# Kernel tuning notes

Measured on AMD Instinct MI355X. Metric: run time of the kernel, lower is better.

Reference implementation:

```python
import jax, jax.numpy as jnp
import numpy as np

NG = 1024      # graphs
NPG = 128      # nodes per graph (forced by lin1 = Linear(128*hid, 128))
N = NG * NPG   # 131072 nodes
DEG = 16       # avg in-graph degree
E = N * DEG    # 2,097,152 edges
IN, H = 4, 64


def setup_inputs() -> dict:
    key = jax.random.key(0)
    ks = jax.random.split(key, 24)
    x = jax.random.normal(ks[0], (N, IN), jnp.float32)
    # edges constrained within each 128-node graph
    src = jax.random.randint(ks[1], (E,), 0, NPG)
    dst = jax.random.randint(ks[2], (E,), 0, NPG)
    off = jnp.repeat(jnp.arange(NG, dtype=jnp.int32) * NPG, NPG * DEG)
    edge_index = jnp.stack([src.astype(jnp.int32) + off, dst.astype(jnp.int32) + off])
    g = lambda k, shp, fan: jax.random.normal(k, shp, jnp.float32) / np.float32(np.sqrt(fan))
    return {
        "x": x, "edge_index": edge_index,
        # GATv2Conv(4->64)
        "Wl": g(ks[3], (IN, H), IN), "bl": jnp.zeros((H,), jnp.float32),
        "Wr": g(ks[4], (IN, H), IN), "br": jnp.zeros((H,), jnp.float32),
        "att_v2": g(ks[5], (H,), H), "b_v2": jnp.zeros((H,), jnp.float32),
        # GATConv #1 (64->64)
        "Wg1": g(ks[6], (H, H), H), "as1": g(ks[7], (H,), H),
        "ad1": g(ks[8], (H,), H), "bg1": jnp.zeros((H,), jnp.float32),
        # GATConv #2 (64->64)
        "Wg2": g(ks[9], (H, H), H), "as2": g(ks[10], (H,), H),
        "ad2": g(ks[11], (H,), H), "bg2": jnp.zeros((H,), jnp.float32),
        # LayerNorm(64)
        "ln_g": jnp.ones((H,), jnp.float32), "ln_b": jnp.zeros((H,), jnp.float32),
        # heads: Linear(128*64 -> 128), Linear(128 -> 1)
        "W1": g(ks[12], (NPG * H, 128), NPG * H), "b1": jnp.zeros((128,), jnp.float32),
        "W2": g(ks[13], (128, 1), 128), "b2": jnp.zeros((1,), jnp.float32),
    }


def _seg_softmax(logits, seg):
    # stable softmax over edges grouped by destination node
    m = jax.ops.segment_max(logits, seg, num_segments=N)
    ex = jnp.exp(logits - m[seg])
    s = jax.ops.segment_sum(ex, seg, num_segments=N)
    return ex / (s[seg] + 1e-16)


def _gatv2(x, src, dst, Wl, bl, Wr, br, att, bias):
    xl = x @ Wl + bl                       # source transform [N,H]
    xr = x @ Wr + br                       # target transform [N,H]
    e = jax.nn.leaky_relu(xl[src] + xr[dst], 0.2) @ att   # [E]
    a = _seg_softmax(e, dst)
    out = jax.ops.segment_sum(a[:, None] * xl[src], dst, num_segments=N)
    return out + bias


def _gat(x, src, dst, W, a_src, a_dst, bias):
    # GATConv default: add self-loops
    loop = jnp.arange(N, dtype=src.dtype)
    s2 = jnp.concatenate([src, loop]); d2 = jnp.concatenate([dst, loop])
    xw = x @ W                             # [N,H]
    al_s = xw @ a_src; al_d = xw @ a_dst   # per-node attention halves [N]
    e = jax.nn.leaky_relu(al_s[s2] + al_d[d2], 0.2)
    a = _seg_softmax(e, d2)
    out = jax.ops.segment_sum(a[:, None] * xw[s2], d2, num_segments=N)
    return out + bias


def _layernorm(x, g, b, eps=1e-5):
    mu = jnp.mean(x, -1, keepdims=True)
    var = jnp.mean(jnp.square(x - mu), -1, keepdims=True)
    return (x - mu) * jax.lax.rsqrt(var + eps) * g + b


def reference(x, edge_index, Wl, bl, Wr, br, att_v2, b_v2,
              Wg1, as1, ad1, bg1, Wg2, as2, ad2, bg2,
              ln_g, ln_b, W1, b1, W2, b2):
    src, dst = edge_index[0], edge_index[1]
    h = jax.nn.leaky_relu(_gatv2(x, src, dst, Wl, bl, Wr, br, att_v2, b_v2), 0.01)
    h = _layernorm(h, ln_g, ln_b)
    h = jax.nn.relu(_gat(h, src, dst, Wg1, as1, ad1, bg1))
    h = jax.nn.relu(_gat(h, src, dst, Wg2, as2, ad2, bg2))
    # linearize: batch is sorted with exactly NPG nodes per graph -> reshape
    h = h.reshape(NG, NPG * H)
    h = jax.nn.leaky_relu(h @ W1 + b1, 0.01)
    return jax.nn.sigmoid(h @ W2 + b2)     # [NG, 1]
```

## Files before the change

kernel.cpp:

```cpp
#include <hip/hip_runtime.h>
#include <hip/hip_bf16.h>

#define NGRAPH 1024
#define NPG 128
#define EPG 2048
#define ETOT (NGRAPH*NPG*16)

typedef unsigned int uint;
typedef unsigned short ushort_t;
typedef __attribute__((ext_vector_type(8))) short s8v;
typedef __attribute__((ext_vector_type(4))) float f32x4;

#define MFMA16 __builtin_amdgcn_mfma_f32_16x16x32_bf16

__device__ __forceinline__ float lrelu(float x, float s){ return fmaxf(x, x*s); }
__device__ __forceinline__ float b2lo(uint u){ return __uint_as_float(u << 16); }
__device__ __forceinline__ float b2hi(uint u){ return __uint_as_float(u & 0xFFFF0000u); }
__device__ __forceinline__ uint pkbf(float a, float b){
  union { __hip_bfloat162 h; uint u; } t;
  t.h = __hip_bfloat162{__float2bfloat16(a), __float2bfloat16(b)};
  return t.u;
}
__device__ __forceinline__ ushort_t bfb(float v){
  union { __hip_bfloat16 h; ushort_t u; } t; t.h = __float2bfloat16(v); return t.u;
}
union U4S8 { uint4 u; s8v s; };
__device__ __forceinline__ s8v bcs8(uint4 u){ U4S8 t; t.u = u; return t.s; }
#define DPP_ADD(v, ctrl) ((v) + __int_as_float(__builtin_amdgcn_update_dpp(0, __float_as_int(v), (ctrl), 0xF, 0xF, false)))

__device__ __forceinline__ int oswz(int r, int p){ return (r<<5) | ((((p>>2) ^ (r & 7))<<2) | (p & 3)); }
__device__ __forceinline__ int obase(int r, int oc){ return (r<<5) | (((oc) ^ (r & 7))<<2); }

__device__ __forceinline__ void fma8(float* acc, uint4 q, float a){
  acc[0] += a*b2lo(q.x); acc[1] += a*b2hi(q.x);
  acc[2] += a*b2lo(q.y); acc[3] += a*b2hi(q.y);
  acc[4] += a*b2lo(q.z); acc[5] += a*b2hi(q.z);
  acc[6] += a*b2lo(q.w); acc[7] += a*b2hi(q.w);
}

#define O_A   0
#define O_B   4096
#define O_EVA 8192
#define O_ED  10240
#define O_WS  11264
#define O_SOF 11392
#define O_ALS 11457
#define O_ALD 11585
#define SM_SZ 11713

__global__ __launch_bounds__(256, 3) void gnn_fused(
    const float* __restrict__ x, const int* __restrict__ ei,
    const float* __restrict__ Wl, const float* __restrict__ bl,
    const float* __restrict__ Wr, const float* __restrict__ br,
    const float* __restrict__ att, const float* __restrict__ bv2,
    const float* __restrict__ Wg1, const float* __restrict__ as1,
    const float* __restrict__ ad1, const float* __restrict__ bg1,
    const float* __restrict__ Wg2, const float* __restrict__ as2,
    const float* __restrict__ ad2, const float* __restrict__ bg2,
    const float* __restrict__ lng, const float* __restrict__ lnb,
    uint* __restrict__ hout)
{
  __shared__ uint SM[SM_SZ];
  float*    eva    = (float*)(SM + O_EVA);
  ushort_t* edsL   = (ushort_t*)(SM + O_ED);
  ushort_t* soff16 = (ushort_t*)(SM + O_SOF);
  float*    als    = (float*)(SM + O_ALS);
  float*    ald    = (float*)(SM + O_ALD);
  float*    was    = (float*)(SM + O_WS);
  float*    wad    = was + 64;
  ushort_t* wgA16  = (ushort_t*)(SM + O_A);
  ushort_t* wg16   = (ushort_t*)(SM + O_EVA);

  const int g    = blockIdx.x;
  const int tid  = threadIdx.x;
  const int lane = tid & 63;
  const int wv   = tid >> 6;
  const int lw   = lane & 15;
  const int lq   = lane >> 4;
  const int sl   = lane & 7;
  const int grp  = lane >> 3;
  const int ebase = g * EPG;

  {
    int* spos = (int*)(SM + O_EVA);
    if (tid < NPG) spos[tid] = 0;
    __syncthreads();
    for (int e = tid; e < EPG; e += 256)
      atomicAdd(&spos[ei[ETOT + ebase + e] - g*NPG], 1);
    __syncthreads();
    if (wv == 0) {
      int c0 = spos[lane], c1 = spos[lane + 64];
      #pragma unroll
      for (int o = 1; o < 64; o <<= 1) { int t = __shfl_up(c0, o); if (lane >= o) c0 += t; }
      #pragma unroll
      for (int o = 1; o < 64; o <<= 1) { int t = __shfl_up(c1, o); if (lane >= o) c1 += t; }
      int tot0 = __shfl(c0, 63);
      soff16[lane + 1]  = (ushort_t)c0;
      soff16[lane + 65] = (ushort_t)(c1 + tot0);
      if (lane == 0) soff16[0] = 0;
    }
    __syncthreads();
    if (tid < NPG) spos[tid] = soff16[tid];
    __syncthreads();
    for (int e = tid; e < EPG; e += 256) {
      int s = ei[ebase + e] - g*NPG;
      int d = ei[ETOT + ebase + e] - g*NPG;
      int p = atomicAdd(&spos[d], 1);
      edsL[p] = (ushort_t)(s | (d << 8));
    }
  }

  {
    const int pl = lane & 31, hb = lane >> 5;
    const float2 wl0 = *(const float2*)&Wl[0*64 + 2*pl];
    const float2 wl1 = *(const float2*)&Wl[1*64 + 2*pl];
    const float2 wl2 = *(const float2*)&Wl[2*64 + 2*pl];
    const float2 wl3 = *(const float2*)&Wl[3*64 + 2*pl];
    const float2 wr0 = *(const float2*)&Wr[0*64 + 2*pl];
    const float2 wr1 = *(const float2*)&Wr[1*64 + 2*pl];
    const float2 wr2 = *(const float2*)&Wr[2*64 + 2*pl];
    const float2 wr3 = *(const float2*)&Wr[3*64 + 2*pl];
    const float2 blp = *(const float2*)&bl[2*pl];
    const float2 brp = *(const float2*)&br[2*pl];
    const float4* x4 = (const float4*)x + (size_t)g * NPG;
    for (int st = 0; st < 16; st++) {
      int i = st*8 + wv*2 + hb;
      float4 xi = x4[i];
      float l0 = blp.x + xi.x*wl0.x + xi.y*wl1.x + xi.z*wl2.x + xi.w*wl3.x;
      float l1 = blp.y + xi.x*wl0.y + xi.y*wl1.y + xi.z*wl2.y + xi.w*wl3.y;
      float r0 = brp.x + xi.x*wr0.x + xi.y*wr1.x + xi.z*wr2.x + xi.w*wr3.x;
      float r1 = brp.y + xi.x*wr0.y + xi.y*wr1.y + xi.z*wr2.y + xi.w*wr3.y;
      SM[O_A + oswz(i, pl)] = pkbf(l0, l1);
      SM[O_B + oswz(i, pl)] = pkbf(r0, r1);
    }
  }
  __syncthreads();

  {
    float4 atA = *(const float4*)&att[sl*8];
    float4 atB = *(const float4*)&att[sl*8 + 4];
    float4 bvA = *(const float4*)&bv2[sl*8];
    float4 bvB = *(const float4*)&bv2[sl*8 + 4];
    for (int pass = 0; pass < 4; pass++) {
      int d  = wv*32 + pass*8 + grp;
      int p0 = soff16[d], p1 = soff16[d+1];
      uint4 qr = *(uint4*)&SM[O_B + obase(d, sl)];
      float m = -1e30f;
      if (p0 < p1) {
        int sN = edsL[p0] & 127;
        uint4 qN = *(uint4*)&SM[O_A + obase(sN, sl)];
        for (int e = p0; e < p1; e++) {
          uint4 ql = qN;
          if (e + 1 < p1) { sN = edsL[e+1] & 127; qN = *(uint4*)&SM[O_A + obase(sN, sl)]; }
          float pt;
          pt  = lrelu(b2lo(ql.x)+b2lo(qr.x), 0.2f)*atA.x;
          pt += lrelu(b2hi(ql.x)+b2hi(qr.x), 0.2f)*atA.y;
          pt += lrelu(b2lo(ql.y)+b2lo(qr.y), 0.2f)*atA.z;
          pt += lrelu(b2hi(ql.y)+b2hi(qr.y), 0.2f)*atA.w;
          pt += lrelu(b2lo(ql.z)+b2lo(qr.z), 0.2f)*atB.x;
          pt += lrelu(b2hi(ql.z)+b2hi(qr.z), 0.2f)*atB.y;
          pt += lrelu(b2lo(ql.w)+b2lo(qr.w), 0.2f)*atB.z;
          pt += lrelu(b2hi(ql.w)+b2hi(qr.w), 0.2f)*atB.w;
          pt += __shfl_xor(pt, 1); pt += __shfl_xor(pt, 2); pt += __shfl_xor(pt, 4);
          if (sl == 0) eva[e] = pt;
          m = fmaxf(m, pt);
        }
      }
      float ss = 0.f;
      for (int e = p0 + sl; e < p1; e += 8) ss += __expf(eva[e] - m);
      ss += __shfl_xor(ss, 1); ss += __shfl_xor(ss, 2); ss += __shfl_xor(ss, 4);
      float rnm = 1.f / (ss + 1e-16f);
      float acc[8] = {0,0,0,0,0,0,0,0};
      if (p0 < p1) {
        int sN = edsL[p0] & 127;
        uint4 qN = *(uint4*)&SM[O_A + obase(sN, sl)];
        float evN = eva[p0];
        for (int e = p0; e < p1; e++) {
          uint4 ql = qN; float ev = evN;
          if (e + 1 < p1) {
            sN = edsL[e+1] & 127;
            qN = *(uint4*)&SM[O_A + obase(sN, sl)];
            evN = eva[e+1];
          }
          fma8(acc, ql, __expf(ev - m) * rnm);
        }
      }
      uint4 o;
      o.x = pkbf(lrelu(acc[0]+bvA.x,0.01f), lrelu(acc[1]+bvA.y,0.01f));
      o.y = pkbf(lrelu(acc[2]+bvA.z,0.01f), lrelu(acc[3]+bvA.w,0.01f));
      o.z = pkbf(lrelu(acc[4]+bvB.x,0.01f), lrelu(acc[5]+bvB.y,0.01f));
      o.w = pkbf(lrelu(acc[6]+bvB.z,0.01f), lrelu(acc[7]+bvB.w,0.01f));
      *(uint4*)&SM[O_B + obase(d, sl)] = o;
    }
  }
  __syncthreads();

  {
    int pl = lane & 31, hb = lane >> 5;
    float2 gv = *(const float2*)&lng[2*pl];
    float2 bv = *(const float2*)&lnb[2*pl];
    for (int it = 0; it < 16; it++) {
      int d = it*8 + wv*2 + hb;
      uint w = SM[O_B + oswz(d, pl)];
      float v0 = b2lo(w), v1 = b2hi(w);
      float s1 = v0 + v1, s2 = v0*v0 + v1*v1;
      #pragma unroll
      for (int o = 1; o < 32; o <<= 1) { s1 += __shfl_xor(s1, o); s2 += __shfl_xor(s2, o); }
      float mu  = s1 * 0.015625f;
      float var = s2 * 0.015625f - mu*mu;
      float rs  = rsqrtf(var + 1e-5f);
      SM[O_B + oswz(d, pl)] = pkbf((v0-mu)*rs*gv.x + bv.x, (v1-mu)*rs*gv.y + bv.y);
    }
  }
  __syncthreads();

  for (int layer = 0; layer < 2; layer++) {
    const float* Wg  = layer ? Wg2 : Wg1;
    const float* avs = layer ? as2 : as1;
    const float* avd = layer ? ad2 : ad1;
    const float* bg  = layer ? bg2 : bg1;

    if (tid < 128) {
      const float* av = (tid < 64) ? avs : avd;
      float* dst = (tid < 64) ? was : wad;
      int k = tid & 63;
      float acc = 0.f;
      #pragma unroll
      for (int jj = 0; jj < 16; jj++) {
        float4 w = *(const float4*)&Wg[k*64 + jj*4];
        float4 a = *(const float4*)&av[jj*4];
        acc += w.x*a.x + w.y*a.y + w.z*a.z + w.w*a.w;
      }
      dst[k] = acc;
    } else {
      int t2 = tid - 128;
      #pragma unroll
      for (int i = 0; i < 8; i++) {
        int idx = t2 + i*128;
        int k = idx >> 4, j4 = (idx & 15)*4;
        float4 w = *(const float4*)&Wg[k*64 + j4];
        wg16[oswz(j4+0, k>>1)*2 + (k&1)] = bfb(w.x);
        wg16[oswz(j4+1, k>>1)*2 + (k&1)] = bfb(w.y);
        wg16[oswz(j4+2, k>>1)*2 + (k&1)] = bfb(w.z);
        wg16[oswz(j4+3, k>>1)*2 + (k&1)] = bfb(w.w);
      }
    }
    __syncthreads();

    {
      int row = 16*wv + lw;
      s8v a0 = bcs8(*(uint4*)&SM[O_EVA + obase(row, lq)]);
      s8v a1 = bcs8(*(uint4*)&SM[O_EVA + obase(row, 4+lq)]);
      int j0 = 16*wv + lq*4;
      #pragma unroll
      for (int nt = 0; nt < 8; nt++) {
        int d = nt*16 + lw;
        s8v b0 = bcs8(*(uint4*)&SM[O_B + obase(d, lq)]);
        s8v b1 = bcs8(*(uint4*)&SM[O_B + obase(d, 4+lq)]);
        f32x4 c = {0.f,0.f,0.f,0.f};
        c = MFMA16(a0, b0, c, 0, 0, 0);
        c = MFMA16(a1, b1, c, 0, 0, 0);
        #pragma unroll
        for (int rg = 0; rg < 4; rg++) {
          int j = j0 + rg;
          wgA16[oswz(d, j>>1)*2 + (j&1)] = bfb(c[rg]);
        }
      }
      float4 ws0 = *(float4*)&was[sl*8], ws1 = *(float4*)&was[sl*8 + 4];
      float4 wd0 = *(float4*)&wad[sl*8], wd1 = *(float4*)&wad[sl*8 + 4];
      for (int ps = 0; ps < 4; ps++) {
        int n = ps*32 + (tid >> 3);
        uint4 q = *(uint4*)&SM[O_B + obase(n, sl)];
        float f0=b2lo(q.x), f1=b2hi(q.x), f2=b2lo(q.y), f3=b2hi(q.y);
        float f4=b2lo(q.z), f5=b2hi(q.z), f6=b2lo(q.w), f7=b2hi(q.w);
        float sa = f0*ws0.x+f1*ws0.y+f2*ws0.z+f3*ws0.w+f4*ws1.x+f5*ws1.y+f6*ws1.z+f7*ws1.w;
        float sd = f0*wd0.x+f1*wd0.y+f2*wd0.z+f3*wd0.w+f4*wd1.x+f5*wd1.y+f6*wd1.z+f7*wd1.w;
        sa = DPP_ADD(sa, 0x111); sa = DPP_ADD(sa, 0x112); sa = DPP_ADD(sa, 0x114);
        sd = DPP_ADD(sd, 0x111); sd = DPP_ADD(sd, 0x112); sd = DPP_ADD(sd, 0x114);
        if ((lane & 7) == 7) { als[n] = sa; ald[n] = sd; }
      }
    }
    __syncthreads();

    {
      float4 bgA = *(const float4*)&bg[sl*8];
      float4 bgB = *(const float4*)&bg[sl*8 + 4];
      for (int pass = 0; pass < 4; pass++) {
        int d  = wv*32 + pass*8 + grp;
        int p0 = soff16[d], p1 = soff16[d+1];
        float ald_d = ald[d];
        float lgs = lrelu(als[d] + ald_d, 0.2f);
        float m = lgs;
        for (int e = p0 + sl; e < p1; e += 8)
          m = fmaxf(m, lrelu(als[edsL[e] & 127] + ald_d, 0.2f));
        m = fmaxf(m, __shfl_xor(m, 1)); m = fmaxf(m, __shfl_xor(m, 2)); m = fmaxf(m, __shfl_xor(m, 4));
        float ex0 = __expf(lgs - m);
        float ss = (sl == 0) ? ex0 : 0.f;
        for (int e = p0 + sl; e < p1; e += 8)
          ss += __expf(lrelu(als[edsL[e] & 127] + ald_d, 0.2f) - m);
        ss += __shfl_xor(ss, 1); ss += __shfl_xor(ss, 2); ss += __shfl_xor(ss, 4);
        float rnm = 1.f / (ss + 1e-16f);
        float acc[8] = {0,0,0,0,0,0,0,0};
        fma8(acc, *(uint4*)&SM[O_A + obase(d, sl)], ex0 * rnm);
        if (p0 < p1) {
          int sN = edsL[p0] & 127;
          float alN = als[sN];
          uint4 qN = *(uint4*)&SM[O_A + obase(sN, sl)];
          for (int e = p0; e < p1; e++) {
            uint4 ql = qN; float alv = alN;
            if (e + 1 < p1) {
              sN = edsL[e+1] & 127;
              alN = als[sN];
              qN = *(uint4*)&SM[O_A + obase(sN, sl)];
            }
            fma8(acc, ql, __expf(lrelu(alv + ald_d, 0.2f) - m) * rnm);
          }
        }
        uint4 o;
        o.x = pkbf(fmaxf(acc[0]+bgA.x,0.f), fmaxf(acc[1]+bgA.y,0.f));
        o.y = pkbf(fmaxf(acc[2]+bgA.z,0.f), fmaxf(acc[3]+bgA.w,0.f));
        o.z = pkbf(fmaxf(acc[4]+bgB.x,0.f), fmaxf(acc[5]+bgB.y,0.f));
        o.w = pkbf(fmaxf(acc[6]+bgB.z,0.f), fmaxf(acc[7]+bgB.w,0.f));
        *(uint4*)&SM[O_B + obase(d, sl)] = o;
      }
    }
    __syncthreads();
  }

  {
    uint* hg = hout + (size_t)g * 4096;
    #pragma unroll
    for (int i = 0; i < 16; i++) {
      int idx = tid + i*256;
      hg[idx] = SM[O_B + oswz(idx >> 5, idx & 31)];
    }
  }
}

__global__ __launch_bounds__(256) void w1_transpose(const float* __restrict__ W1,
                                                    uint* __restrict__ w1t)
{
  __shared__ float sw[64*130];
  const int tid = threadIdx.x;
  const int k0 = blockIdx.x * 64;
  #pragma unroll
  for (int i = 0; i < 8; i++) {
    int idx = tid + i*256;
    int r = idx >> 5, c4 = (idx & 31)*4;
    *(float4*)&sw[r*130 + c4] = *(const float4*)&W1[(size_t)(k0+r)*128 + c4];
  }
  __syncthreads();
  #pragma unroll
  for (int i = 0; i < 16; i++) {
    int idx = tid + i*256;
    int c = idx >> 5, kp = idx & 31;
    w1t[(size_t)c*4096 + (k0>>1) + kp] = pkbf(sw[(2*kp)*130 + c], sw[(2*kp+1)*130 + c]);
  }
}

__global__ __launch_bounds__(256) void head_gemm(
    const uint* __restrict__ hbuf, const uint* __restrict__ w1t,
    float* __restrict__ partial)
{
  __shared__ uint sAh[2048];
  __shared__ uint sBh[4096];
  const int tid = threadIdx.x, lane = tid & 63, wv = tid >> 6;
  const int lw = lane & 15, lq = lane >> 4;
  const int g0 = blockIdx.x * 64;
  const int ks = blockIdx.y;
  f32x4 acc[8];
  #pragma unroll
  for (int i = 0; i < 8; i++) acc[i] = f32x4{0.f,0.f,0.f,0.f};

  for (int ch = 0; ch < 8; ch++) {
    int pb = ks*256 + ch*32;
    #pragma unroll
    for (int i = 0; i < 2; i++) {
      int idx = tid + i*256; int r = idx >> 3, q4 = idx & 7;
      uint4 v = *(const uint4*)&hbuf[(size_t)(g0+r)*4096 + pb + q4*4];
      *(uint4*)&sAh[(r<<5) | ((q4 ^ (r & 7))<<2)] = v;
    }
    #pragma unroll
    for (int i = 0; i < 4; i++) {
      int idx = tid + i*256; int r = idx >> 3, q4 = idx & 7;
      uint4 v = *(const uint4*)&w1t[(size_t)r*4096 + pb + q4*4];
      *(uint4*)&sBh[(r<<5) | ((q4 ^ (r & 7))<<2)] = v;
    }
    __syncthreads();
    int ra = 16*wv + lw;
    s8v a0 = bcs8(*(uint4*)&sAh[obase(ra, lq)]);
    s8v a1 = bcs8(*(uint4*)&sAh[obase(ra, 4+lq)]);
    #pragma unroll
    for (int nt = 0; nt < 8; nt++) {
      int c = nt*16 + lw;
      s8v b0 = bcs8(*(uint4*)&sBh[obase(c, lq)]);
      s8v b1 = bcs8(*(uint4*)&sBh[obase(c, 4+lq)]);
      acc[nt] = MFMA16(a0, b0, acc[nt], 0, 0, 0);
      acc[nt] = MFMA16(a1, b1, acc[nt], 0, 0, 0);
    }
    __syncthreads();
  }
  float* pp = partial + (size_t)ks*131072;
  #pragma unroll
  for (int nt = 0; nt < 8; nt++) {
    int c = nt*16 + lw;
    int r0 = g0 + 16*wv + lq*4;
    #pragma unroll
    for (int rg = 0; rg < 4; rg++)
      pp[(size_t)(r0+rg)*128 + c] = acc[nt][rg];
  }
}

__global__ __launch_bounds__(256) void head_out(
    const float* __restrict__ partial, const float* __restrict__ b1,
    const float* __restrict__ W2, const float* __restrict__ b2,
    float* __restrict__ out)
{
  const int tid = threadIdx.x;
  const int gl  = tid >> 5;
  const int c4  = tid & 31;
  const int g   = blockIdx.x*8 + gl;
  float4 v = *(const float4*)&b1[c4*4];
  #pragma unroll
  for (int s = 0; s < 16; s++) {
    float4 p = *(const float4*)&partial[(size_t)s*131072 + (size_t)g*128 + c4*4];
    v.x += p.x; v.y += p.y; v.z += p.z; v.w += p.w;
  }
  float4 w = *(const float4*)&W2[c4*4];
  float t = lrelu(v.x,0.01f)*w.x + lrelu(v.y,0.01f)*w.y
          + lrelu(v.z,0.01f)*w.z + lrelu(v.w,0.01f)*w.w;
  #pragma unroll
  for (int m = 1; m < 32; m <<= 1) t += __shfl_xor(t, m);
  if (c4 == 0) out[g] = 1.f / (1.f + __expf(-(t + b2[0])));
}

extern "C" void kernel_launch(void* const* d_in, const int* in_sizes, int n_in,
                              void* d_out, int out_size, void* d_ws, size_t ws_size,
                              hipStream_t stream) {
  const float* x   = (const float*)d_in[0];
  const int*   ei  = (const int*)  d_in[1];
  const float* Wl  = (const float*)d_in[2];
  const float* bl_ = (const float*)d_in[3];
  const float* Wr  = (const float*)d_in[4];
  const float* br_ = (const float*)d_in[5];
  const float* att = (const float*)d_in[6];
  const float* bv2 = (const float*)d_in[7];
  const float* Wg1 = (const float*)d_in[8];
  const float* as1 = (const float*)d_in[9];
  const float* ad1 = (const float*)d_in[10];
  const float* bg1 = (const float*)d_in[11];
  const float* Wg2 = (const float*)d_in[12];
  const float* as2 = (const float*)d_in[13];
  const float* ad2 = (const float*)d_in[14];
  const float* bg2 = (const float*)d_in[15];
  const float* lng = (const float*)d_in[16];
  const float* lnb = (const float*)d_in[17];
  const float* W1  = (const float*)d_in[18];
  const float* b1  = (const float*)d_in[19];
  const float* W2  = (const float*)d_in[20];
  const float* b2  = (const float*)d_in[21];
  float* out = (float*)d_out;

  uint*  hbuf    = (uint*)d_ws;
  float* partial = (float*)((char*)d_ws + (size_t)16*1024*1024);
  uint*  w1t     = (uint*)((char*)d_ws + (size_t)24*1024*1024);

  w1_transpose<<<128, 256, 0, stream>>>(W1, w1t);
  gnn_fused<<<NGRAPH, 256, 0, stream>>>(x, ei, Wl, bl_, Wr, br_, att, bv2,
      Wg1, as1, ad1, bg1, Wg2, as2, ad2, bg2, lng, lnb, hbuf);
  head_gemm<<<dim3(16, 16), 256, 0, stream>>>(hbuf, w1t, partial);
  head_out<<<128, 256, 0, stream>>>(partial, b1, W2, b2, out);
}
```

Measured before the change: 314.7 us.

## Switch GNN to fp16 with dot2, edge-parallel attention logits, drop W1 transpose kernel

Moves all intermediate storage and MFMA inputs from bf16 to fp16, so packed fp16 math (fdot2, half2 add and mul) can compute the GATv2 logits, the LayerNorm sums and the attention halves. Attention logits are now computed edge-parallel across all threads into a shared buffer. A separate segment-softmax pass then stores exponentials and per-node reciprocal sums, so the aggregation loops only do weighted FMAs and apply the normalizer once at the end. The separate W1 transpose kernel is removed and head_gemm converts and transposes W1 from fp32 itself on every tile load, trading a launch for strided global reads. fp16 has narrower range than bf16, which adds a risk of overflow or accuracy loss.

```diff
diff --git a/kernel.cpp b/kernel.cpp
--- a/kernel.cpp
+++ b/kernel.cpp
@@ -1,5 +1,6 @@
 #include <hip/hip_runtime.h>
 #include <hip/hip_bf16.h>
+#include <hip/hip_fp16.h>
 
 #define NGRAPH 1024
 #define NPG 128
@@ -8,34 +9,50 @@
 
 typedef unsigned int uint;
 typedef unsigned short ushort_t;
-typedef __attribute__((ext_vector_type(8))) short s8v;
+typedef __attribute__((ext_vector_type(2))) _Float16 h2v;
+typedef __attribute__((ext_vector_type(8))) _Float16 h8v;
 typedef __attribute__((ext_vector_type(4))) float f32x4;
 
-#define MFMA16 __builtin_amdgcn_mfma_f32_16x16x32_bf16
+#define MFMA16H __builtin_amdgcn_mfma_f32_16x16x32_f16
+#define FDOT2(a,b,c) __builtin_amdgcn_fdot2((a),(b),(c),false)
+
+union U1H2 { uint u; h2v h; };
+union U4H8 { uint4 u; h8v h; };
+union U4H2 { uint4 u; h2v h[4]; };
 
 __device__ __forceinline__ float lrelu(float x, float s){ return fmaxf(x, x*s); }
-__device__ __forceinline__ float b2lo(uint u){ return __uint_as_float(u << 16); }
-__device__ __forceinline__ float b2hi(uint u){ return __uint_as_float(u & 0xFFFF0000u); }
-__device__ __forceinline__ uint pkbf(float a, float b){
-  union { __hip_bfloat162 h; uint u; } t;
-  t.h = __hip_bfloat162{__float2bfloat16(a), __float2bfloat16(b)};
-  return t.u;
-}
-__device__ __forceinline__ ushort_t bfb(float v){
-  union { __hip_bfloat16 h; ushort_t u; } t; t.h = __float2bfloat16(v); return t.u;
-}
-union U4S8 { uint4 u; s8v s; };
-__device__ __forceinline__ s8v bcs8(uint4 u){ U4S8 t; t.u = u; return t.s; }
+__device__ __forceinline__ uint pkh(float a, float b){
+  U1H2 t; t.h.x = (_Float16)a; t.h.y = (_Float16)b; return t.u;
+}
+__device__ __forceinline__ ushort_t hfb(float v){
+  union { _Float16 h; ushort_t u; } t; t.h = (_Float16)v; return t.u;
+}
+__device__ __forceinline__ float2 uph(uint u){
+  U1H2 t; t.u = u;
+  return float2{(float)t.h.x, (float)t.h.y};
+}
 #define DPP_ADD(v, ctrl) ((v) + __int_as_float(__builtin_amdgcn_update_dpp(0, __float_as_int(v), (ctrl), 0xF, 0xF, false)))
 
 __device__ __forceinline__ int oswz(int r, int p){ return (r<<5) | ((((p>>2) ^ (r & 7))<<2) | (p & 3)); }
 __device__ __forceinline__ int obase(int r, int oc){ return (r<<5) | (((oc) ^ (r & 7))<<2); }
 
 __device__ __forceinline__ void fma8(float* acc, uint4 q, float a){
-  acc[0] += a*b2lo(q.x); acc[1] += a*b2hi(q.x);
-  acc[2] += a*b2lo(q.y); acc[3] += a*b2hi(q.y);
-  acc[4] += a*b2lo(q.z); acc[5] += a*b2hi(q.z);
-  acc[6] += a*b2lo(q.w); acc[7] += a*b2hi(q.w);
+  float2 f0 = uph(q.x), f1 = uph(q.y), f2 = uph(q.z), f3 = uph(q.w);
+  acc[0] += a*f0.x; acc[1] += a*f0.y;
+  acc[2] += a*f1.x; acc[3] += a*f1.y;
+  acc[4] += a*f2.x; acc[5] += a*f2.y;
+  acc[6] += a*f3.x; acc[7] += a*f3.y;
+}
+
+__device__ __forceinline__ float dotp(uint ul, uint ur, h2v a2, float acc){
+  U1H2 l, r; l.u = ul; r.u = ur;
+  h2v v = l.h + r.h;
+  U1H2 sv; sv.h = v;
+  U1H2 av; av.u = sv.u & 0x7FFF7FFFu;
+  h2v c6; c6.x = (_Float16)0.6f; c6.y = (_Float16)0.6f;
+  h2v c4; c4.x = (_Float16)0.4f; c4.y = (_Float16)0.4f;
+  h2v w = v * c6 + av.h * c4;
+  return FDOT2(w, a2, acc);
 }
 
 #define O_A   0
@@ -130,66 +147,87 @@
       float l1 = blp.y + xi.x*wl0.y + xi.y*wl1.y + xi.z*wl2.y + xi.w*wl3.y;
       float r0 = brp.x + xi.x*wr0.x + xi.y*wr1.x + xi.z*wr2.x + xi.w*wr3.x;
       float r1 = brp.y + xi.x*wr0.y + xi.y*wr1.y + xi.z*wr2.y + xi.w*wr3.y;
-      SM[O_A + oswz(i, pl)] = pkbf(l0, l1);
-      SM[O_B + oswz(i, pl)] = pkbf(r0, r1);
+      SM[O_A + oswz(i, pl)] = pkh(l0, l1);
+      SM[O_B + oswz(i, pl)] = pkh(r0, r1);
     }
   }
   __syncthreads();
 
   {
-    float4 atA = *(const float4*)&att[sl*8];
-    float4 atB = *(const float4*)&att[sl*8 + 4];
-    float4 bvA = *(const float4*)&bv2[sl*8];
-    float4 bvB = *(const float4*)&bv2[sl*8 + 4];
+    h2v att2[32];
+    #pragma unroll
+    for (int p2 = 0; p2 < 32; p2++) {
+      att2[p2].x = (_Float16)att[2*p2];
+      att2[p2].y = (_Float16)att[2*p2 + 1];
+    }
+    for (int it = 0; it < 8; it++) {
+      int e  = tid + it*256;
+      int sd = edsL[e];
+      int s  = sd & 127, d = sd >> 8;
+      float acc = 0.f;
+      #pragma unroll
+      for (int c = 0; c < 8; c++) {
+        uint4 ql = *(uint4*)&SM[O_A + obase(s, c)];
+        uint4 qr = *(uint4*)&SM[O_B + obase(d, c)];
+        acc = dotp(ql.x, qr.x, att2[4*c+0], acc);
+        acc = dotp(ql.y, qr.y, att2[4*c+1], acc);
+        acc = dotp(ql.z, qr.z, att2[4*c+2], acc);
+        acc = dotp(ql.w, qr.w, att2[4*c+3], acc);
+      }
+      eva[e] = acc;
+    }
+  }
+  __syncthreads();
+
+  {
+    const int dd = tid >> 4, sl16 = tid & 15;
+    for (int it = 0; it < 8; it++) {
+      int d = it*16 + dd;
+      int p0 = soff16[d], p1 = soff16[d+1];
+      float m = -1e30f;
+      for (int p = p0 + sl16; p < p1; p += 16) m = fmaxf(m, eva[p]);
+      #pragma unroll
+      for (int o = 1; o < 16; o <<= 1) m = fmaxf(m, __shfl_xor(m, o));
+      float ss = 0.f;
+      for (int p = p0 + sl16; p < p1; p += 16) {
+        float ex = __expf(eva[p] - m); ss += ex; eva[p] = ex;
+      }
+      #pragma unroll
+      for (int o = 1; o < 16; o <<= 1) ss += __shfl_xor(ss, o);
+      if (sl16 == 0) als[d] = 1.f / (ss + 1e-16f);
+    }
+  }
+  __syncthreads();
+
+  {
+    float2 bvA = *(const float2*)&bv2[sl*8];
+    float2 bvB = *(const float2*)&bv2[sl*8 + 2];
+    float2 bvC = *(const float2*)&bv2[sl*8 + 4];
+    float2 bvD = *(const float2*)&bv2[sl*8 + 6];
     for (int pass = 0; pass < 4; pass++) {
       int d  = wv*32 + pass*8 + grp;
       int p0 = soff16[d], p1 = soff16[d+1];
-      uint4 qr = *(uint4*)&SM[O_B + obase(d, sl)];
-      float m = -1e30f;
-      if (p0 < p1) {
-        int sN = edsL[p0] & 127;
-        uint4 qN = *(uint4*)&SM[O_A + obase(sN, sl)];
-        for (int e = p0; e < p1; e++) {
-          uint4 ql = qN;
-          if (e + 1 < p1) { sN = edsL[e+1] & 127; qN = *(uint4*)&SM[O_A + obase(sN, sl)]; }
-          float pt;
-          pt  = lrelu(b2lo(ql.x)+b2lo(qr.x), 0.2f)*atA.x;
-          pt += lrelu(b2hi(ql.x)+b2hi(qr.x), 0.2f)*atA.y;
-          pt += lrelu(b2lo(ql.y)+b2lo(qr.y), 0.2f)*atA.z;
-          pt += lrelu(b2hi(ql.y)+b2hi(qr.y), 0.2f)*atA.w;
-          pt += lrelu(b2lo(ql.z)+b2lo(qr.z), 0.2f)*atB.x;
-          pt += lrelu(b2hi(ql.z)+b2hi(qr.z), 0.2f)*atB.y;
-          pt += lrelu(b2lo(ql.w)+b2lo(qr.w), 0.2f)*atB.z;
-          pt += lrelu(b2hi(ql.w)+b2hi(qr.w), 0.2f)*atB.w;
-          pt += __shfl_xor(pt, 1); pt += __shfl_xor(pt, 2); pt += __shfl_xor(pt, 4);
-          if (sl == 0) eva[e] = pt;
-          m = fmaxf(m, pt);
-        }
-      }
-      float ss = 0.f;
-      for (int e = p0 + sl; e < p1; e += 8) ss += __expf(eva[e] - m);
-      ss += __shfl_xor(ss, 1); ss += __shfl_xor(ss, 2); ss += __shfl_xor(ss, 4);
-      float rnm = 1.f / (ss + 1e-16f);
       float acc[8] = {0,0,0,0,0,0,0,0};
       if (p0 < p1) {
         int sN = edsL[p0] & 127;
         uint4 qN = *(uint4*)&SM[O_A + obase(sN, sl)];
-        float evN = eva[p0];
+        float wN = eva[p0];
         for (int e = p0; e < p1; e++) {
-          uint4 ql = qN; float ev = evN;
+          uint4 ql = qN; float w = wN;
           if (e + 1 < p1) {
             sN = edsL[e+1] & 127;
             qN = *(uint4*)&SM[O_A + obase(sN, sl)];
-            evN = eva[e+1];
+            wN = eva[e+1];
           }
-          fma8(acc, ql, __expf(ev - m) * rnm);
+          fma8(acc, ql, w);
         }
       }
+      float nm = als[d];
       uint4 o;
-      o.x = pkbf(lrelu(acc[0]+bvA.x,0.01f), lrelu(acc[1]+bvA.y,0.01f));
-      o.y = pkbf(lrelu(acc[2]+bvA.z,0.01f), lrelu(acc[3]+bvA.w,0.01f));
-      o.z = pkbf(lrelu(acc[4]+bvB.x,0.01f), lrelu(acc[5]+bvB.y,0.01f));
-      o.w = pkbf(lrelu(acc[6]+bvB.z,0.01f), lrelu(acc[7]+bvB.w,0.01f));
+      o.x = pkh(lrelu(acc[0]*nm+bvA.x,0.01f), lrelu(acc[1]*nm+bvA.y,0.01f));
+      o.y = pkh(lrelu(acc[2]*nm+bvB.x,0.01f), lrelu(acc[3]*nm+bvB.y,0.01f));
+      o.z = pkh(lrelu(acc[4]*nm+bvC.x,0.01f), lrelu(acc[5]*nm+bvC.y,0.01f));
+      o.w = pkh(lrelu(acc[6]*nm+bvD.x,0.01f), lrelu(acc[7]*nm+bvD.y,0.01f));
       *(uint4*)&SM[O_B + obase(d, sl)] = o;
     }
   }
@@ -199,17 +237,20 @@
     int pl = lane & 31, hb = lane >> 5;
     float2 gv = *(const float2*)&lng[2*pl];
     float2 bv = *(const float2*)&lnb[2*pl];
+    h2v one2; one2.x = (_Float16)1.f; one2.y = (_Float16)1.f;
     for (int it = 0; it < 16; it++) {
       int d = it*8 + wv*2 + hb;
       uint w = SM[O_B + oswz(d, pl)];
-      float v0 = b2lo(w), v1 = b2hi(w);
-      float s1 = v0 + v1, s2 = v0*v0 + v1*v1;
+      U1H2 t; t.u = w;
+      float s1 = FDOT2(t.h, one2, 0.f);
+      float s2 = FDOT2(t.h, t.h, 0.f);
       #pragma unroll
       for (int o = 1; o < 32; o <<= 1) { s1 += __shfl_xor(s1, o); s2 += __shfl_xor(s2, o); }
       float mu  = s1 * 0.015625f;
       float var = s2 * 0.015625f - mu*mu;
       float rs  = rsqrtf(var + 1e-5f);
-      SM[O_B + oswz(d, pl)] = pkbf((v0-mu)*rs*gv.x + bv.x, (v1-mu)*rs*gv.y + bv.y);
+      float2 f = uph(w);
+      SM[O_B + oswz(d, pl)] = pkh((f.x-mu)*rs*gv.x + bv.x, (f.y-mu)*rs*gv.y + bv.y);
     }
   }
   __syncthreads();
@@ -239,42 +280,51 @@
         int idx = t2 + i*128;
         int k = idx >> 4, j4 = (idx & 15)*4;
         float4 w = *(const float4*)&Wg[k*64 + j4];
-        wg16[oswz(j4+0, k>>1)*2 + (k&1)] = bfb(w.x);
-        wg16[oswz(j4+1, k>>1)*2 + (k&1)] = bfb(w.y);
-        wg16[oswz(j4+2, k>>1)*2 + (k&1)] = bfb(w.z);
-        wg16[oswz(j4+3, k>>1)*2 + (k&1)] = bfb(w.w);
+        wg16[oswz(j4+0, k>>1)*2 + (k&1)] = hfb(w.x);
+        wg16[oswz(j4+1, k>>1)*2 + (k&1)] = hfb(w.y);
+        wg16[oswz(j4+2, k>>1)*2 + (k&1)] = hfb(w.z);
+        wg16[oswz(j4+3, k>>1)*2 + (k&1)] = hfb(w.w);
       }
     }
     __syncthreads();
 
     {
-      int row = 16*wv + lw;
-      s8v a0 = bcs8(*(uint4*)&SM[O_EVA + obase(row, lq)]);
-      s8v a1 = bcs8(*(uint4*)&SM[O_EVA + obase(row, 4+lq)]);
+      U4H8 a0t, a1t;
+      a0t.u = *(uint4*)&SM[O_EVA + obase(16*wv + lw, lq)];
+      a1t.u = *(uint4*)&SM[O_EVA + obase(16*wv + lw, 4+lq)];
       int j0 = 16*wv + lq*4;
       #pragma unroll
       for (int nt = 0; nt < 8; nt++) {
         int d = nt*16 + lw;
-        s8v b0 = bcs8(*(uint4*)&SM[O_B + obase(d, lq)]);
-        s8v b1 = bcs8(*(uint4*)&SM[O_B + obase(d, 4+lq)]);
+        U4H8 b0t, b1t;
+        b0t.u = *(uint4*)&SM[O_B + obase(d, lq)];
+        b1t.u = *(uint4*)&SM[O_B + obase(d, 4+lq)];
         f32x4 c = {0.f,0.f,0.f,0.f};
-        c = MFMA16(a0, b0, c, 0, 0, 0);
-        c = MFMA16(a1, b1, c, 0, 0, 0);
+        c = MFMA16H(a0t.h, b0t.h, c, 0, 0, 0);
+        c = MFMA16H(a1t.h, b1t.h, c, 0, 0, 0);
         #pragma unroll
         for (int rg = 0; rg < 4; rg++) {
           int j = j0 + rg;
-          wgA16[oswz(d, j>>1)*2 + (j&1)] = bfb(c[rg]);
+          wgA16[oswz(d, j>>1)*2 + (j&1)] = hfb(c[rg]);
         }
       }
-      float4 ws0 = *(float4*)&was[sl*8], ws1 = *(float4*)&was[sl*8 + 4];
-      float4 wd0 = *(float4*)&wad[sl*8], wd1 = *(float4*)&wad[sl*8 + 4];
+      h2v ws2[4], wd2[4];
+      #pragma unroll
+      for (int q2 = 0; q2 < 4; q2++) {
+        float2 a = *(float2*)&was[sl*8 + 2*q2];
+        float2 b = *(float2*)&wad[sl*8 + 2*q2];
+        ws2[q2].x = (_Float16)a.x; ws2[q2].y = (_Float16)a.y;
+        wd2[q2].x = (_Float16)b.x; wd2[q2].y = (_Float16)b.y;
+      }
       for (int ps = 0; ps < 4; ps++) {
         int n = ps*32 + (tid >> 3);
-        uint4 q = *(uint4*)&SM[O_B + obase(n, sl)];
-        float f0=b2lo(q.x), f1=b2hi(q.x), f2=b2lo(q.y), f3=b2hi(q.y);
-        float f4=b2lo(q.z), f5=b2hi(q.z), f6=b2lo(q.w), f7=b2hi(q.w);
-        float sa = f0*ws0.x+f1*ws0.y+f2*ws0.z+f3*ws0.w+f4*ws1.x+f5*ws1.y+f6*ws1.z+f7*ws1.w;
-        float sd = f0*wd0.x+f1*wd0.y+f2*wd0.z+f3*wd0.w+f4*wd1.x+f5*wd1.y+f6*wd1.z+f7*wd1.w;
+        U4H2 q; q.u = *(uint4*)&SM[O_B + obase(n, sl)];
+        float sa = 0.f, sd = 0.f;
+        #pragma unroll
+        for (int q2 = 0; q2 < 4; q2++) {
+          sa = FDOT2(q.h[q2], ws2[q2], sa);
+          sd = FDOT2(q.h[q2], wd2[q2], sd);
+        }
         sa = DPP_ADD(sa, 0x111); sa = DPP_ADD(sa, 0x112); sa = DPP_ADD(sa, 0x114);
         sd = DPP_ADD(sd, 0x111); sd = DPP_ADD(sd, 0x112); sd = DPP_ADD(sd, 0x114);
         if ((lane & 7) == 7) { als[n] = sa; ald[n] = sd; }
@@ -282,45 +332,68 @@
     }
     __syncthreads();
 
+    for (int it = 0; it < 8; it++) {
+      int e  = tid + it*256;
+      int sd = edsL[e];
+      eva[e] = lrelu(als[sd & 127] + ald[sd >> 8], 0.2f);
+    }
+    __syncthreads();
+
     {
-      float4 bgA = *(const float4*)&bg[sl*8];
-      float4 bgB = *(const float4*)&bg[sl*8 + 4];
+      const int dd = tid >> 4, sl16 = tid & 15;
+      for (int it = 0; it < 8; it++) {
+        int d = it*16 + dd;
+        int p0 = soff16[d], p1 = soff16[d+1];
+        float lgs = lrelu(als[d] + ald[d], 0.2f);
+        float m = lgs;
+        for (int p = p0 + sl16; p < p1; p += 16) m = fmaxf(m, eva[p]);
+        #pragma unroll
+        for (int o = 1; o < 16; o <<= 1) m = fmaxf(m, __shfl_xor(m, o));
+        float ex0 = __expf(lgs - m);
+        float ss = 0.f;
+        for (int p = p0 + sl16; p < p1; p += 16) {
+          float ex = __expf(eva[p] - m); ss += ex; eva[p] = ex;
+        }
+        #pragma unroll
+        for (int o = 1; o < 16; o <<= 1) ss += __shfl_xor(ss, o);
+        if (sl16 == 0) {
+          als[d] = ex0;
+          ald[d] = 1.f / (ss + ex0 + 1e-16f);
+        }
+      }
+    }
+    __syncthreads();
+
+    {
+      float2 bgA = *(const float2*)&bg[sl*8];
+      float2 bgB = *(const float2*)&bg[sl*8 + 2];
+      float2 bgC = *(const float2*)&bg[sl*8 + 4];
+      float2 bgD = *(const float2*)&bg[sl*8 + 6];
       for (int pass = 0; pass < 4; pass++) {
         int d  = wv*32 + pass*8 + grp;
         int p0 = soff16[d], p1 = soff16[d+1];
-        float ald_d = ald[d];
-        float lgs = lrelu(als[d] + ald_d, 0.2f);
-        float m = lgs;
-        for (int e = p0 + sl; e < p1; e += 8)
-          m = fmaxf(m, lrelu(als[edsL[e] & 127] + ald_d, 0.2f));
-        m = fmaxf(m, __shfl_xor(m, 1)); m = fmaxf(m, __shfl_xor(m, 2)); m = fmaxf(m, __shfl_xor(m, 4));
-        float ex0 = __expf(lgs - m);
-        float ss = (sl == 0) ? ex0 : 0.f;
-        for (int e = p0 + sl; e < p1; e += 8)
-          ss += __expf(lrelu(als[edsL[e] & 127] + ald_d, 0.2f) - m);
-        ss += __shfl_xor(ss, 1); ss += __shfl_xor(ss, 2); ss += __shfl_xor(ss, 4);
-        float rnm = 1.f / (ss + 1e-16f);
         float acc[8] = {0,0,0,0,0,0,0,0};
-        fma8(acc, *(uint4*)&SM[O_A + obase(d, sl)], ex0 * rnm);
+        fma8(acc, *(uint4*)&SM[O_A + obase(d, sl)], als[d]);
         if (p0 < p1) {
           int sN = edsL[p0] & 127;
-          float alN = als[sN];
           uint4 qN = *(uint4*)&SM[O_A + obase(sN, sl)];
+          float wN = eva[p0];
           for (int e = p0; e < p1; e++) {
-            uint4 ql = qN; float alv = alN;
+            uint4 ql = qN; float w = wN;
             if (e + 1 < p1) {
               sN = edsL[e+1] & 127;
-              alN = als[sN];
               qN = *(uint4*)&SM[O_A + obase(sN, sl)];
+              wN = eva[e+1];
             }
-            fma8(acc, ql, __expf(lrelu(alv + ald_d, 0.2f) - m) * rnm);
+            fma8(acc, ql, w);
           }
         }
+        float nm = ald[d];
         uint4 o;
-        o.x = pkbf(fmaxf(acc[0]+bgA.x,0.f), fmaxf(acc[1]+bgA.y,0.f));
-        o.y = pkbf(fmaxf(acc[2]+bgA.z,0.f), fmaxf(acc[3]+bgA.w,0.f));
-        o.z = pkbf(fmaxf(acc[4]+bgB.x,0.f), fmaxf(acc[5]+bgB.y,0.f));
-        o.w = pkbf(fmaxf(acc[6]+bgB.z,0.f), fmaxf(acc[7]+bgB.w,0.f));
+        o.x = pkh(fmaxf(acc[0]*nm+bgA.x,0.f), fmaxf(acc[1]*nm+bgA.y,0.f));
+        o.y = pkh(fmaxf(acc[2]*nm+bgB.x,0.f), fmaxf(acc[3]*nm+bgB.y,0.f));
+        o.z = pkh(fmaxf(acc[4]*nm+bgC.x,0.f), fmaxf(acc[5]*nm+bgC.y,0.f));
+        o.w = pkh(fmaxf(acc[6]*nm+bgD.x,0.f), fmaxf(acc[7]*nm+bgD.y,0.f));
         *(uint4*)&SM[O_B + obase(d, sl)] = o;
       }
     }
@@ -337,29 +410,8 @@
   }
 }
 
-__global__ __launch_bounds__(256) void w1_transpose(const float* __restrict__ W1,
-                                                    uint* __restrict__ w1t)
-{
-  __shared__ float sw[64*130];
-  const int tid = threadIdx.x;
-  const int k0 = blockIdx.x * 64;
-  #pragma unroll
-  for (int i = 0; i < 8; i++) {
-    int idx = tid + i*256;
-    int r = idx >> 5, c4 = (idx & 31)*4;
-    *(float4*)&sw[r*130 + c4] = *(const float4*)&W1[(size_t)(k0+r)*128 + c4];
-  }
-  __syncthreads();
-  #pragma unroll
-  for (int i = 0; i < 16; i++) {
-    int idx = tid + i*256;
-    int c = idx >> 5, kp = idx & 31;
-    w1t[(size_t)c*4096 + (k0>>1) + kp] = pkbf(sw[(2*kp)*130 + c], sw[(2*kp+1)*130 + c]);
-  }
-}
-
 __global__ __launch_bounds__(256) void head_gemm(
-    const uint* __restrict__ hbuf, const uint* __restrict__ w1t,
+    const uint* __restrict__ hbuf, const float* __restrict__ W1,
     float* __restrict__ partial)
 {
   __shared__ uint sAh[2048];
@@ -373,7 +425,8 @@
   for (int i = 0; i < 8; i++) acc[i] = f32x4{0.f,0.f,0.f,0.f};
 
   for (int ch = 0; ch < 8; ch++) {
-    int pb = ks*256 + ch*32;
+    int pb  = ks*256 + ch*32;
+    int kk0 = ks*512 + ch*64;
     #pragma unroll
     for (int i = 0; i < 2; i++) {
       int idx = tid + i*256; int r = idx >> 3, q4 = idx & 7;
@@ -381,22 +434,24 @@
       *(uint4*)&sAh[(r<<5) | ((q4 ^ (r & 7))<<2)] = v;
     }
     #pragma unroll
-    for (int i = 0; i < 4; i++) {
-      int idx = tid + i*256; int r = idx >> 3, q4 = idx & 7;
-      uint4 v = *(const uint4*)&w1t[(size_t)r*4096 + pb + q4*4];
-      *(uint4*)&sBh[(r<<5) | ((q4 ^ (r & 7))<<2)] = v;
-    }
-    __syncthreads();
-    int ra = 16*wv + lw;
-    s8v a0 = bcs8(*(uint4*)&sAh[obase(ra, lq)]);
-    s8v a1 = bcs8(*(uint4*)&sAh[obase(ra, 4+lq)]);
+    for (int i = 0; i < 16; i++) {
+      int idx = tid + i*256;
+      int c = idx & 127, kp = idx >> 7;
+      int kk = kk0 + 2*kp;
+      sBh[oswz(c, kp)] = pkh(W1[(size_t)kk*128 + c], W1[(size_t)(kk+1)*128 + c]);
+    }
+    __syncthreads();
+    U4H8 a0t, a1t;
+    a0t.u = *(uint4*)&sAh[obase(16*wv + lw, lq)];
+    a1t.u = *(uint4*)&sAh[obase(16*wv + lw, 4+lq)];
     #pragma unroll
     for (int nt = 0; nt < 8; nt++) {
       int c = nt*16 + lw;
-      s8v b0 = bcs8(*(uint4*)&sBh[obase(c, lq)]);
-      s8v b1 = bcs8(*(uint4*)&sBh[obase(c, 4+lq)]);
-      acc[nt] = MFMA16(a0, b0, acc[nt], 0, 0, 0);
-      acc[nt] = MFMA16(a1, b1, acc[nt], 0, 0, 0);
+      U4H8 b0t, b1t;
+      b0t.u = *(uint4*)&sBh[obase(c, lq)];
+      b1t.u = *(uint4*)&sBh[obase(c, 4+lq)];
+      acc[nt] = MFMA16H(a0t.h, b0t.h, acc[nt], 0, 0, 0);
+      acc[nt] = MFMA16H(a1t.h, b1t.h, acc[nt], 0, 0, 0);
     }
     __syncthreads();
   }
@@ -463,11 +518,9 @@
 
   uint*  hbuf    = (uint*)d_ws;
   float* partial = (float*)((char*)d_ws + (size_t)16*1024*1024);
-  uint*  w1t     = (uint*)((char*)d_ws + (size_t)24*1024*1024);
-
-  w1_transpose<<<128, 256, 0, stream>>>(W1, w1t);
+
   gnn_fused<<<NGRAPH, 256, 0, stream>>>(x, ei, Wl, bl_, Wr, br_, att, bv2,
       Wg1, as1, ad1, bg1, Wg2, as2, ad2, bg2, lng, lnb, hbuf);
-  head_gemm<<<dim3(16, 16), 256, 0, stream>>>(hbuf, w1t, partial);
+  head_gemm<<<dim3(16, 16), 256, 0, stream>>>(hbuf, W1, partial);
   head_out<<<128, 256, 0, stream>>>(partial, b1, W2, b2, out);
 }
```

Result: no change. 310.2 us (-1.5%).
